# Kernel tuning notes

Hardware: AMD Instinct MI355X
Metric: run time of the kernel (lower is better)

Reference implementation:

```python
import jax, jax.numpy as jnp
import numpy as np

B, S, P, D = 32, 512, 512, 768

def setup_inputs() -> dict:
    key = jax.random.key(0)
    k1, k2 = jax.random.split(key)
    inputs = jax.random.normal(k1, (B, S, D), dtype=jnp.float32)
    prototypes = jax.random.normal(k2, (P, D), dtype=jnp.float32)
    return {"inputs": inputs, "prototypes": prototypes}

def reference(inputs, prototypes):
    # Squared Euclidean distance from every token vector to every prototype:
    # but the cross term is a GEMM and the huge [B,S,P,D] intermediate is never built).
    x_sq = jnp.sum(inputs * inputs, axis=-1, keepdims=True)          # [B, S, 1]
    p_sq = jnp.sum(prototypes * prototypes, axis=-1)                 # [P]
    cross = jnp.einsum('bsd,pd->bsp', inputs, prototypes)            # [B, S, P]
    distances = x_sq + p_sq[None, None, :] - 2.0 * cross             # [B, S, P]
    return (distances, prototypes)
```

## Files before the change

kernel.cpp:

```cpp
#include <hip/hip_runtime.h>
#include <hip/hip_bf16.h>


#define M_TOK 16384
#define N_PROT 512
#define K_DIM 768
#define BK 32
#define NCH (K_DIM / BK)
#define ASTR (K_DIM + 8)

typedef __attribute__((ext_vector_type(4))) float f32x4;
typedef __attribute__((ext_vector_type(8))) short bf16x8;

__device__ inline unsigned short f2bf(float f) {
    unsigned int u = __float_as_uint(f);
    u += 0x7fffu + ((u >> 16) & 1u);
    return (unsigned short)(u >> 16);
}

__global__ __launch_bounds__(256) void prep_b(
    const float* __restrict__ p,
    unsigned short* __restrict__ b_bf, float* __restrict__ p_sq,
    float* __restrict__ proto_out)
{
    const int row  = blockIdx.x * 4 + (threadIdx.x >> 6);
    const int lane = threadIdx.x & 63;

    const int g    = row >> 4;
    const int l16p = row & 15;

    const float4* src4 = (const float4*)(p + (size_t)row * K_DIM);
    float4* pout4 = (float4*)(proto_out + (size_t)row * K_DIM);

    float ssum = 0.0f;
#pragma unroll
    for (int j = 0; j < 3; ++j) {
        const int idx = lane + j * 64;
        float4 v = src4[idx];
        ssum += v.x * v.x + v.y * v.y + v.z * v.z + v.w * v.w;
        ushort4 b;
        b.x = f2bf(v.x); b.y = f2bf(v.y); b.z = f2bf(v.z); b.w = f2bf(v.w);
        const int k0   = idx * 4;
        const int kk   = k0 >> 5;
        const int quad = (k0 >> 3) & 3;
        const int j0   = k0 & 7;
        const int dst  = (g * 24 + kk) * 512 + quad * 128 + l16p * 8 + j0;
        *(ushort4*)&b_bf[dst] = b;
        pout4[idx] = v;
    }
#pragma unroll
    for (int off = 32; off > 0; off >>= 1) ssum += __shfl_down(ssum, off);
    if (lane == 0) p_sq[row] = ssum;
}

__global__ __launch_bounds__(512, 2) void dist_main(
    const float* __restrict__ X,
    const unsigned short* __restrict__ Bb,
    const float* __restrict__ p_sq,
    float* __restrict__ out)
{
    __shared__ unsigned short lds_a[64 * ASTR];
    __shared__ float lds_xsq[64];

    const int tid  = threadIdx.x;
    const int wave = tid >> 6;
    const int lane = tid & 63;
    const int bm   = blockIdx.x << 6;
    const int wn   = wave << 6;
    const int quad = lane >> 4;
    const int l16  = lane & 15;

    const int ar = tid >> 3;
    const int ac = tid & 7;
    const float* aptr = X + (size_t)(bm + ar) * K_DIM;
    float asq = 0.0f;
#pragma unroll
    for (int j = 0; j < 24; ++j) {
        const int c4 = ac + 8 * j;
        float4 v = *(const float4*)(aptr + (size_t)c4 * 4);
        asq += v.x * v.x + v.y * v.y + v.z * v.z + v.w * v.w;
        ushort4 u;
        u.x = f2bf(v.x); u.y = f2bf(v.y); u.z = f2bf(v.z); u.w = f2bf(v.w);
        *(ushort4*)&lds_a[ar * ASTR + c4 * 4] = u;
    }
#pragma unroll
    for (int off = 1; off < 8; off <<= 1) asq += __shfl_xor(asq, off);
    if (ac == 0) lds_xsq[ar] = asq;

    __syncthreads();

    const f32x4 zero = {0.0f, 0.0f, 0.0f, 0.0f};
    f32x4 acc[4][4];
#pragma unroll
    for (int mt = 0; mt < 4; ++mt)
#pragma unroll
        for (int nt = 0; nt < 4; ++nt) acc[mt][nt] = zero;

    const unsigned short* bp = Bb + (size_t)lane * 8;
    const int gbase = (wave << 2) * 24;

    bf16x8 bcur[4], bnxt[4];
#pragma unroll
    for (int nt = 0; nt < 4; ++nt)
        bcur[nt] = *(const bf16x8*)(bp + (size_t)(gbase + nt * 24) * 512);

    for (int kc = 0; kc < NCH; ++kc) {
        const int k0 = kc * BK;
        if (kc + 1 < NCH) {
#pragma unroll
            for (int nt = 0; nt < 4; ++nt)
                bnxt[nt] = *(const bf16x8*)(bp
                    + (size_t)(gbase + nt * 24 + kc + 1) * 512);
        }

        bf16x8 af[4];
#pragma unroll
        for (int mt = 0; mt < 4; ++mt)
            af[mt] = *(const bf16x8*)&lds_a[(mt * 16 + l16) * ASTR + k0 + quad * 8];

#pragma unroll
        for (int mt = 0; mt < 4; ++mt)
#pragma unroll
            for (int nt = 0; nt < 4; ++nt)
                acc[mt][nt] = __builtin_amdgcn_mfma_f32_16x16x32_bf16(
                    af[mt], bcur[nt], acc[mt][nt], 0, 0, 0);

#pragma unroll
        for (int nt = 0; nt < 4; ++nt) bcur[nt] = bnxt[nt];
    }

    float ps[4];
#pragma unroll
    for (int nt = 0; nt < 4; ++nt) ps[nt] = p_sq[wn + nt * 16 + l16];

#pragma unroll
    for (int mt = 0; mt < 4; ++mt) {
#pragma unroll
        for (int i = 0; i < 4; ++i) {
            const int lr = mt * 16 + quad * 4 + i;
            const float xs = lds_xsq[lr];
            float* orow = out + (size_t)(bm + lr) * N_PROT + wn + l16;
#pragma unroll
            for (int nt = 0; nt < 4; ++nt)
                orow[nt * 16] = xs + ps[nt] - 2.0f * acc[mt][nt][i];
        }
    }
}

extern "C" void kernel_launch(void* const* d_in, const int* in_sizes, int n_in,
                              void* d_out, int out_size, void* d_ws, size_t ws_size,
                              hipStream_t stream) {
    const float* inputs = (const float*)d_in[0];
    const float* protos = (const float*)d_in[1];
    float* out = (float*)d_out;
    float* proto_out = out + (size_t)M_TOK * N_PROT;

    char* ws = (char*)d_ws;
    unsigned short* b_bf = (unsigned short*)ws;
    float* p_sq = (float*)(ws + 786432);

    prep_b<<<128, 256, 0, stream>>>(protos, b_bf, p_sq, proto_out);
    dist_main<<<M_TOK / 64, 512, 0, stream>>>(inputs, b_bf, p_sq, out);
}
```

Measured before the change: 102.6 us.

## Pipeline A-tile global loads and bf16 conversion with MFMA compute across K windows

Instead of loading and converting the whole 64x768 A tile into LDS before any MFMA work, the K dimension is split into 8 windows of 3 chunks. The next window's A values and B fragments are prefetched into registers while the current window's MFMAs run, then converted and written to LDS. This aims to hide global-load latency behind compute. In exchange it adds a barrier per window and doubles the B register buffers, which raises register pressure and could lower occupancy.

```diff
diff --git a/kernel.cpp b/kernel.cpp
--- a/kernel.cpp
+++ b/kernel.cpp
@@ -6,7 +6,8 @@
 #define N_PROT 512
 #define K_DIM 768
 #define BK 32
-#define NCH (K_DIM / BK)
+#define NW 8
+#define SPW 3
 #define ASTR (K_DIM + 8)
 
 typedef __attribute__((ext_vector_type(4))) float f32x4;
@@ -73,9 +74,11 @@
     const int ar = tid >> 3;
     const int ac = tid & 7;
     const float* aptr = X + (size_t)(bm + ar) * K_DIM;
+
     float asq = 0.0f;
+
 #pragma unroll
-    for (int j = 0; j < 24; ++j) {
+    for (int j = 0; j < 3; ++j) {
         const int c4 = ac + 8 * j;
         float4 v = *(const float4*)(aptr + (size_t)c4 * 4);
         asq += v.x * v.x + v.y * v.y + v.z * v.z + v.w * v.w;
@@ -83,11 +86,10 @@
         u.x = f2bf(v.x); u.y = f2bf(v.y); u.z = f2bf(v.z); u.w = f2bf(v.w);
         *(ushort4*)&lds_a[ar * ASTR + c4 * 4] = u;
     }
-#pragma unroll
-    for (int off = 1; off < 8; off <<= 1) asq += __shfl_xor(asq, off);
-    if (ac == 0) lds_xsq[ar] = asq;
+    __syncthreads();
 
-    __syncthreads();
+    const unsigned short* bp = Bb + (size_t)lane * 8;
+    const int gbase = (wave << 2) * 24;
 
     const f32x4 zero = {0.0f, 0.0f, 0.0f, 0.0f};
     f32x4 acc[4][4];
@@ -96,38 +98,69 @@
 #pragma unroll
         for (int nt = 0; nt < 4; ++nt) acc[mt][nt] = zero;
 
-    const unsigned short* bp = Bb + (size_t)lane * 8;
-    const int gbase = (wave << 2) * 24;
+    bf16x8 bw[SPW][4], bn[SPW][4];
+#pragma unroll
+    for (int s = 0; s < SPW; ++s)
+#pragma unroll
+        for (int nt = 0; nt < 4; ++nt)
+            bw[s][nt] = *(const bf16x8*)(bp + (size_t)(gbase + nt * 24 + s) * 512);
 
-    bf16x8 bcur[4], bnxt[4];
 #pragma unroll
-    for (int nt = 0; nt < 4; ++nt)
-        bcur[nt] = *(const bf16x8*)(bp + (size_t)(gbase + nt * 24) * 512);
+    for (int w = 0; w < NW; ++w) {
+        if (w + 1 < NW) {
+#pragma unroll
+            for (int s = 0; s < SPW; ++s)
+#pragma unroll
+                for (int nt = 0; nt < 4; ++nt)
+                    bn[s][nt] = *(const bf16x8*)(bp
+                        + (size_t)(gbase + nt * 24 + (w + 1) * SPW + s) * 512);
+        }
+        float4 sv[3];
+        if (w + 1 < NW) {
+#pragma unroll
+            for (int j = 0; j < 3; ++j)
+                sv[j] = *(const float4*)(aptr
+                    + (size_t)((w + 1) * 24 + ac + 8 * j) * 4);
+        }
+        __builtin_amdgcn_sched_barrier(0);
 
-    for (int kc = 0; kc < NCH; ++kc) {
-        const int k0 = kc * BK;
-        if (kc + 1 < NCH) {
 #pragma unroll
-            for (int nt = 0; nt < 4; ++nt)
-                bnxt[nt] = *(const bf16x8*)(bp
-                    + (size_t)(gbase + nt * 24 + kc + 1) * 512);
+        for (int s = 0; s < SPW; ++s) {
+            const int k0 = (w * SPW + s) * BK;
+            bf16x8 af[4];
+#pragma unroll
+            for (int mt = 0; mt < 4; ++mt)
+                af[mt] = *(const bf16x8*)&lds_a[(mt * 16 + l16) * ASTR + k0 + quad * 8];
+#pragma unroll
+            for (int mt = 0; mt < 4; ++mt)
+#pragma unroll
+                for (int nt = 0; nt < 4; ++nt)
+                    acc[mt][nt] = __builtin_amdgcn_mfma_f32_16x16x32_bf16(
+                        af[mt], bw[s][nt], acc[mt][nt], 0, 0, 0);
         }
 
-        bf16x8 af[4];
+        if (w + 1 < NW) {
 #pragma unroll
-        for (int mt = 0; mt < 4; ++mt)
-            af[mt] = *(const bf16x8*)&lds_a[(mt * 16 + l16) * ASTR + k0 + quad * 8];
+            for (int j = 0; j < 3; ++j) {
+                float4 v = sv[j];
+                asq += v.x * v.x + v.y * v.y + v.z * v.z + v.w * v.w;
+                ushort4 u;
+                u.x = f2bf(v.x); u.y = f2bf(v.y); u.z = f2bf(v.z); u.w = f2bf(v.w);
+                *(ushort4*)&lds_a[ar * ASTR + ((w + 1) * 24 + ac + 8 * j) * 4] = u;
+            }
+            __syncthreads();
+#pragma unroll
+            for (int s = 0; s < SPW; ++s)
+#pragma unroll
+                for (int nt = 0; nt < 4; ++nt)
+                    bw[s][nt] = bn[s][nt];
+        }
+    }
 
 #pragma unroll
-        for (int mt = 0; mt < 4; ++mt)
-#pragma unroll
-            for (int nt = 0; nt < 4; ++nt)
-                acc[mt][nt] = __builtin_amdgcn_mfma_f32_16x16x32_bf16(
-                    af[mt], bcur[nt], acc[mt][nt], 0, 0, 0);
-
-#pragma unroll
-        for (int nt = 0; nt < 4; ++nt) bcur[nt] = bnxt[nt];
-    }
+    for (int off = 1; off < 8; off <<= 1) asq += __shfl_xor(asq, off);
+    if (ac == 0) lds_xsq[ar] = asq;
+    __syncthreads();
 
     float ps[4];
 #pragma unroll
```

Result: slower. 114.4 us (+11.4%).

## Split dist_main into producer waves feeding MFMA waves via LDS chunk flags

Applied to the files above, without the earlier changes.

Adds four producer waves per block that load and convert X chunks to bf16 in LDS, computing row norms with LDS atomics and signalling per-K-chunk ready flags. The eight MFMA waves spin on these flags so the GEMM can start before the whole A tile is staged, overlapping global loads with compute. This costs larger blocks, tighter register limits from the new launch bounds, and busy-wait spinning on LDS flags.

```diff
diff --git a/kernel.cpp b/kernel.cpp
--- a/kernel.cpp
+++ b/kernel.cpp
@@ -53,7 +53,7 @@
     if (lane == 0) p_sq[row] = ssum;
 }
 
-__global__ __launch_bounds__(512, 2) void dist_main(
+__global__ __launch_bounds__(768, 3) void dist_main(
     const float* __restrict__ X,
     const unsigned short* __restrict__ Bb,
     const float* __restrict__ p_sq,
@@ -61,88 +61,121 @@
 {
     __shared__ unsigned short lds_a[64 * ASTR];
     __shared__ float lds_xsq[64];
+    __shared__ unsigned flags[NCH];
 
     const int tid  = threadIdx.x;
     const int wave = tid >> 6;
     const int lane = tid & 63;
     const int bm   = blockIdx.x << 6;
-    const int wn   = wave << 6;
-    const int quad = lane >> 4;
-    const int l16  = lane & 15;
 
-    const int ar = tid >> 3;
-    const int ac = tid & 7;
-    const float* aptr = X + (size_t)(bm + ar) * K_DIM;
-    float asq = 0.0f;
+    if (tid < NCH) flags[tid] = 0u;
+    if (tid < 64)  lds_xsq[tid] = 0.0f;
+    __syncthreads();
+
+    f32x4 acc[4][4];
+
+    if (wave < 8) {
+        const int quad = lane >> 4;
+        const int l16  = lane & 15;
+
+        const unsigned short* bp = Bb + (size_t)lane * 8;
+        const int gbase = (wave << 2) * 24;
+
+        const f32x4 zero = {0.0f, 0.0f, 0.0f, 0.0f};
 #pragma unroll
-    for (int j = 0; j < 24; ++j) {
-        const int c4 = ac + 8 * j;
-        float4 v = *(const float4*)(aptr + (size_t)c4 * 4);
-        asq += v.x * v.x + v.y * v.y + v.z * v.z + v.w * v.w;
-        ushort4 u;
-        u.x = f2bf(v.x); u.y = f2bf(v.y); u.z = f2bf(v.z); u.w = f2bf(v.w);
-        *(ushort4*)&lds_a[ar * ASTR + c4 * 4] = u;
+        for (int mt = 0; mt < 4; ++mt)
+#pragma unroll
+            for (int nt = 0; nt < 4; ++nt) acc[mt][nt] = zero;
+
+        bf16x8 bcur[4], bnxt[4];
+#pragma unroll
+        for (int nt = 0; nt < 4; ++nt)
+            bcur[nt] = *(const bf16x8*)(bp + (size_t)(gbase + nt * 24) * 512);
+
+        volatile unsigned* vf = flags;
+        for (int kc = 0; kc < NCH; ++kc) {
+            while (vf[kc] == 0u) { }
+
+            const int k0 = kc * BK;
+            if (kc + 1 < NCH) {
+#pragma unroll
+                for (int nt = 0; nt < 4; ++nt)
+                    bnxt[nt] = *(const bf16x8*)(bp
+                        + (size_t)(gbase + nt * 24 + kc + 1) * 512);
+            }
+
+            bf16x8 af[4];
+#pragma unroll
+            for (int mt = 0; mt < 4; ++mt)
+                af[mt] = *(const bf16x8*)&lds_a[(mt * 16 + l16) * ASTR + k0 + quad * 8];
+
+#pragma unroll
+            for (int mt = 0; mt < 4; ++mt)
+#pragma unroll
+                for (int nt = 0; nt < 4; ++nt)
+                    acc[mt][nt] = __builtin_amdgcn_mfma_f32_16x16x32_bf16(
+                        af[mt], bcur[nt], acc[mt][nt], 0, 0, 0);
+
+#pragma unroll
+            for (int nt = 0; nt < 4; ++nt) bcur[nt] = bnxt[nt];
+        }
+    } else {
+        const int pw = wave - 8;
+        const int pr = lane >> 3;
+        const int pc = lane & 7;
+        float asqp[8] = {0, 0, 0, 0, 0, 0, 0, 0};
+
+        for (int s = 0; s < 6; ++s) {
+            const int kc = pw + 4 * s;
+            const float* base = X + (size_t)bm * K_DIM + (size_t)(kc * 8 + pc) * 4;
+            float4 v[8];
+#pragma unroll
+            for (int i = 0; i < 8; ++i)
+                v[i] = *(const float4*)(base + (size_t)(i * 8 + pr) * K_DIM);
+#pragma unroll
+            for (int i = 0; i < 8; ++i) {
+                float4 x = v[i];
+                asqp[i] += x.x * x.x + x.y * x.y + x.z * x.z + x.w * x.w;
+                ushort4 u;
+                u.x = f2bf(x.x); u.y = f2bf(x.y); u.z = f2bf(x.z); u.w = f2bf(x.w);
+                *(ushort4*)&lds_a[(i * 8 + pr) * ASTR + (kc * 8 + pc) * 4] = u;
+            }
+            __threadfence_block();
+            ((volatile unsigned*)flags)[kc] = 1u;
+        }
+
+#pragma unroll
+        for (int i = 0; i < 8; ++i) {
+            float t = asqp[i];
+            t += __shfl_xor(t, 1);
+            t += __shfl_xor(t, 2);
+            t += __shfl_xor(t, 4);
+            if (pc == 0) atomicAdd(&lds_xsq[i * 8 + pr], t);
+        }
     }
-#pragma unroll
-    for (int off = 1; off < 8; off <<= 1) asq += __shfl_xor(asq, off);
-    if (ac == 0) lds_xsq[ar] = asq;
 
     __syncthreads();
 
-    const f32x4 zero = {0.0f, 0.0f, 0.0f, 0.0f};
-    f32x4 acc[4][4];
+    if (wave < 8) {
+        const int quad = lane >> 4;
+        const int l16  = lane & 15;
+        const int wn   = wave << 6;
+
+        float ps[4];
 #pragma unroll
-    for (int mt = 0; mt < 4; ++mt)
-#pragma unroll
-        for (int nt = 0; nt < 4; ++nt) acc[mt][nt] = zero;
-
-    const unsigned short* bp = Bb + (size_t)lane * 8;
-    const int gbase = (wave << 2) * 24;
-
-    bf16x8 bcur[4], bnxt[4];
-#pragma unroll
-    for (int nt = 0; nt < 4; ++nt)
-        bcur[nt] = *(const bf16x8*)(bp + (size_t)(gbase + nt * 24) * 512);
-
-    for (int kc = 0; kc < NCH; ++kc) {
-        const int k0 = kc * BK;
-        if (kc + 1 < NCH) {
-#pragma unroll
-            for (int nt = 0; nt < 4; ++nt)
-                bnxt[nt] = *(const bf16x8*)(bp
-                    + (size_t)(gbase + nt * 24 + kc + 1) * 512);
-        }
-
-        bf16x8 af[4];
-#pragma unroll
-        for (int mt = 0; mt < 4; ++mt)
-            af[mt] = *(const bf16x8*)&lds_a[(mt * 16 + l16) * ASTR + k0 + quad * 8];
+        for (int nt = 0; nt < 4; ++nt) ps[nt] = p_sq[wn + nt * 16 + l16];
 
 #pragma unroll
-        for (int mt = 0; mt < 4; ++mt)
+        for (int mt = 0; mt < 4; ++mt) {
 #pragma unroll
-            for (int nt = 0; nt < 4; ++nt)
-                acc[mt][nt] = __builtin_amdgcn_mfma_f32_16x16x32_bf16(
-                    af[mt], bcur[nt], acc[mt][nt], 0, 0, 0);
-
+            for (int i = 0; i < 4; ++i) {
+                const int lr = mt * 16 + quad * 4 + i;
+                const float xs = lds_xsq[lr];
+                float* orow = out + (size_t)(bm + lr) * N_PROT + wn + l16;
 #pragma unroll
-        for (int nt = 0; nt < 4; ++nt) bcur[nt] = bnxt[nt];
-    }
-
-    float ps[4];
-#pragma unroll
-    for (int nt = 0; nt < 4; ++nt) ps[nt] = p_sq[wn + nt * 16 + l16];
-
-#pragma unroll
-    for (int mt = 0; mt < 4; ++mt) {
-#pragma unroll
-        for (int i = 0; i < 4; ++i) {
-            const int lr = mt * 16 + quad * 4 + i;
-            const float xs = lds_xsq[lr];
-            float* orow = out + (size_t)(bm + lr) * N_PROT + wn + l16;
-#pragma unroll
-            for (int nt = 0; nt < 4; ++nt)
-                orow[nt * 16] = xs + ps[nt] - 2.0f * acc[mt][nt][i];
+                for (int nt = 0; nt < 4; ++nt)
+                    orow[nt * 16] = xs + ps[nt] - 2.0f * acc[mt][nt][i];
+            }
         }
     }
 }
@@ -160,5 +193,5 @@
     float* p_sq = (float*)(ws + 786432);
 
     prep_b<<<128, 256, 0, stream>>>(protos, b_bf, p_sq, proto_out);
-    dist_main<<<M_TOK / 64, 512, 0, stream>>>(inputs, b_bf, p_sq, out);
+    dist_main<<<M_TOK / 64, 768, 0, stream>>>(inputs, b_bf, p_sq, out);
 }
```

Result: slower. 124.3 us (+21.1%).
